# Kernel tuning notes

Hardware: AMD Instinct MI355X
Metric: run time of the kernel (lower is better)

The kernel has to match this reference:

```python
import jax, jax.numpy as jnp
import numpy as np
from jax import lax

GEN_POLY = ("1111001", "1011011")  # rate 1/2, constraint length 7 (octal 171/133)


def build_trellis(gen_poly):
    """Feed-forward (non-recursive) convolutional trellis tables.

    State = shift-register contents, most-recent bit is the MSB of the state
    index. Returns int32 tables, each [ns, ni]:
      to_nodes[s, b]        : next state from state s with input bit b
      op_by_fromnode[s, b]  : emitted output-symbol index for (s, b)
      from_nodes[j, m]      : m-th predecessor state of state j
      ip_by_tonode[j, m]    : input bit taken on that predecessor transition
    """
    mu = len(gen_poly[0]) - 1
    ns, ni = 2 ** mu, 2
    g = np.array([[int(c) for c in p] for p in gen_poly])  # [conv_n, mu+1]
    to_nodes = np.zeros((ns, ni), np.int32)
    op_by_fromnode = np.zeros((ns, ni), np.int32)
    from_nodes = np.zeros((ns, ni), np.int32)
    ip_by_tonode = np.zeros((ns, ni), np.int32)
    fill = np.zeros(ns, np.int32)
    for s in range(ns):
        rbits = [(s >> (mu - 1 - j)) & 1 for j in range(mu)]
        for b in range(ni):
            w = np.array([b] + rbits)                 # full window [b, r0..r_{mu-1}]
            obits = (g @ w) % 2                        # output bits, MSB first
            o = int("".join(str(int(x)) for x in obits), 2)
            j = int("".join(str(x) for x in ([b] + rbits[:-1])), 2)
            to_nodes[s, b] = j
            op_by_fromnode[s, b] = o
            from_nodes[j, fill[j]] = s
            ip_by_tonode[j, fill[j]] = b
            fill[j] += 1
    return to_nodes, op_by_fromnode, from_nodes, ip_by_tonode


TO_NODES, OP_BY_FROM, FROM_NODES, IP_BY_TO = build_trellis(GEN_POLY)
CONV_N = len(GEN_POLY)
MU = len(GEN_POLY[0]) - 1
NS = 2 ** MU
NO = 2 ** CONV_N
# output-symbol bit patterns, MSB first, mapped to signs (1-2*bit)
_OP_BITS = np.array([[(o >> (CONV_N - 1 - j)) & 1 for j in range(CONV_N)]
                     for o in range(NO)], np.float32)
OP_SIGN = jnp.asarray(1.0 - 2.0 * _OP_BITS)  # [NO, CONV_N]
IP_SIGN = jnp.asarray([1.0, -1.0])           # sign of input bit b: 1-2b


def setup_inputs() -> dict:
    key = jax.random.key(0)
    k1, k2 = jax.random.split(key)
    B, n = 256, 4096
    T = n // CONV_N  # = k = 2048 info bits
    llr_ch = jax.random.normal(k1, (B, n), dtype=jnp.float32)
    llr_a = jax.random.normal(k2, (B, T), dtype=jnp.float32)
    return {"llr_ch": llr_ch, "llr_a": llr_a}


def _bcjr(llr_ch, llr_a):
    B, n = llr_ch.shape
    T = n // CONV_N
    # branch metrics: bm[t, b, o] = exp(0.5 * sum_j llr[b, t, j] * (1-2*opbit_j(o)))
    llr_r = llr_ch.reshape(B, T, CONV_N)
    bm = jnp.exp(0.5 * jnp.einsum('btj,oj->tbo', llr_r, OP_SIGN))  # [T, B, NO]
    llr_a_t = llr_a.T  # [T, B]

    def gamma_fn(bm_t, la_t):
        # a-priori factor exp(0.5*llr_a*(1-2b)) times channel branch metric
        ap = jnp.exp(0.5 * la_t[:, None, None] * IP_SIGN[None, None, :])  # [B,1,2]
        return ap * bm_t[:, OP_BY_FROM]  # [B, NS, 2]

    alpha0 = jnp.zeros((B, NS), jnp.float32).at[:, 0].set(1.0)

    def fwd(alpha_prev, inp):
        bm_t, la_t = inp
        gam = gamma_fn(bm_t, la_t)                        # [B, NS, 2] by from-state
        ag = gam * alpha_prev[:, :, None]                  # alpha_{t} * gamma_t
        agt = ag[:, FROM_NODES, IP_BY_TO]                  # regroup by to-state
        alpha = agt.sum(-1)
        alpha = alpha / alpha.sum(-1, keepdims=True)       # normalize (as in TF code)
        return alpha, alpha_prev                            # emit alpha BEFORE step t

    _, alphas = lax.scan(fwd, alpha0, (bm, llr_a_t))       # alphas[t] = alpha_t, [T,B,NS]

    beta_T = jnp.full((B, NS), 1.0 / NS, jnp.float32)      # non-terminated: uniform

    def bwd(beta_next, inp):
        bm_t, la_t, alpha_t = inp
        gam = gamma_fn(bm_t, la_t)                         # [B, NS, 2]
        bg = gam * beta_next[:, TO_NODES]                  # gamma * beta_{t+1}(to)
        beta = bg.sum(-1)
        beta = beta / beta.sum(-1, keepdims=True)
        joint = alpha_t[:, :, None] * bg                   # APP per (state, bit)
        llr_t = jnp.log(joint[..., 0].sum(-1)) - jnp.log(joint[..., 1].sum(-1))
        return beta, llr_t

    _, llrs_rev = lax.scan(bwd, beta_T, (bm[::-1], llr_a_t[::-1], alphas[::-1]))
    return llrs_rev[::-1].T  # [B, T] soft LLRs (hard_out=False)


def reference(llr_ch, llr_a):
    return _bcjr(llr_ch, llr_a)
```

## Files before the change

### kernel.cpp

```cpp
#include <hip/hip_runtime.h>

#define T_LEN 2048
#define NSTATE 64
#define NCHUNK 32
#define CH_S 64
#define WARM 64
#define RK 16

template<int CTRL>
__device__ __forceinline__ float dpp_add(float v) {
    int r = __builtin_amdgcn_update_dpp(0, __float_as_int(v), CTRL, 0xF, 0xF, true);
    return v + __int_as_float(r);
}

__device__ __forceinline__ float dpp_sum_to63(float v) {
    v = dpp_add<0x111>(v);
    v = dpp_add<0x112>(v);
    v = dpp_add<0x114>(v);
    v = dpp_add<0x118>(v);
    v = dpp_add<0x142>(v);
    v = dpp_add<0x143>(v);
    return v;
}

__device__ __forceinline__ float wave_total(float v) {
    float s = dpp_sum_to63(v);
    return __int_as_float(__builtin_amdgcn_readlane(__float_as_int(s), 63));
}

__device__ __forceinline__ float pair_sum_xor1(float v) {
    int r = __builtin_amdgcn_update_dpp(0, __float_as_int(v), 0xB1, 0xF, 0xF, true);
    return v + __int_as_float(r);
}

__device__ __forceinline__ unsigned short bf16_of(float f) {
    return (unsigned short)((__float_as_uint(f) + 0x8000u) >> 16);
}


template<bool STORE>
__device__ __forceinline__ float fwd_group(float state,
                                           const float* __restrict__ chp,
                                           const float* __restrict__ lap,
                                           unsigned short* __restrict__ alds,
                                           int g, int t0, int lane,
                                           float kE, float k0, float k1,
                                           int fs0, bool fhi)
{
    #pragma unroll
    for (int h = 0; h < 2; ++h) {
        const int gb = g + 8 * h;
        const float4* c4 = (const float4*)(chp + 2 * gb);
        const float4* a4 = (const float4*)(lap + gb);
        float4 cc[4], aa[2];
        #pragma unroll
        for (int i = 0; i < 4; ++i) cc[i] = c4[i];
        #pragma unroll
        for (int i = 0; i < 2; ++i) aa[i] = a4[i];
        #pragma unroll
        for (int i = 0; i < 8; ++i) {
            float l0 = (i & 1) ? cc[i >> 1].z : cc[i >> 1].x;
            float l1 = (i & 1) ? cc[i >> 1].w : cc[i >> 1].y;
            float la = ((const float*)aa)[i];
            if (STORE) alds[(gb + i - t0) * NSTATE + lane] = bf16_of(state);
            float x   = fmaf(la, kE, fmaf(l0, k0, l1 * k1));
            float g0v = exp2f(x);
            float g1v = __builtin_amdgcn_rcpf(g0v);
            float s0  = pair_sum_xor1(state * g0v);
            float s1  = pair_sum_xor1(state * g1v);
            float a0  = __shfl(s0, fs0, 64);
            float a1  = __shfl(s1, fs0, 64);
            state = fhi ? a1 : a0;
        }
    }
    float s = wave_total(state);
    return state * __builtin_amdgcn_rcpf(s);
}

template<bool LLR>
__device__ __forceinline__ float bwd_group(float state,
                                           const float* __restrict__ chp,
                                           const float* __restrict__ lap,
                                           const unsigned short* __restrict__ alds,
                                           float* __restrict__ outp,
                                           int g, int t0, int lane,
                                           float kE, float k0, float k1,
                                           int bs0, int bs1)
{
    #pragma unroll
    for (int h = 1; h >= 0; --h) {
        const int gb = g + 8 * h;
        const float4* c4 = (const float4*)(chp + 2 * gb);
        const float4* a4 = (const float4*)(lap + gb);
        float4 cc[4], aa[2];
        #pragma unroll
        for (int i = 0; i < 4; ++i) cc[i] = c4[i];
        #pragma unroll
        for (int i = 0; i < 2; ++i) aa[i] = a4[i];
        float av[8];
        if (LLR) {
            #pragma unroll
            for (int i = 0; i < 8; ++i)
                av[i] = __uint_as_float(((unsigned)alds[(gb + i - t0) * NSTATE + lane]) << 16);
        }
        #pragma unroll
        for (int i = 7; i >= 0; --i) {
            float l0 = (i & 1) ? cc[i >> 1].z : cc[i >> 1].x;
            float l1 = (i & 1) ? cc[i >> 1].w : cc[i >> 1].y;
            float la = ((const float*)aa)[i];
            float x   = fmaf(la, kE, fmaf(l0, k0, l1 * k1));
            float g0v = exp2f(x);
            float g1v = __builtin_amdgcn_rcpf(g0v);
            float t0v = __shfl(state, bs0, 64);
            float t1v = __shfl(state, bs1, 64);
            float p0 = g0v * t0v;
            float p1 = g1v * t1v;
            if (LLR) {
                float na = dpp_sum_to63(av[i] * p0);
                float nb = dpp_sum_to63(av[i] * p1);
                float d  = (__log2f(na) - __log2f(nb)) * 0.6931471805599453f;
                if (lane == 63) outp[gb + i] = d;
            }
            state = p0 + p1;
        }
    }
    float s = wave_total(state);
    return state * __builtin_amdgcn_rcpf(s);
}

__global__ __launch_bounds__(128, 8)
void bcjr_fused_kernel(const float* __restrict__ llr_ch,
                       const float* __restrict__ llr_a,
                       float* __restrict__ out)
{
    __shared__ unsigned short alds[CH_S * NSTATE];

    const int lane  = threadIdx.x & 63;
    const int role  = threadIdx.x >> 6;
    const int unit  = blockIdx.x;
    const int chunk = unit & (NCHUNK - 1);
    const int b     = unit >> 5;

    const float c0 = 1.0f - 2.0f * (float)(__popc(lane & 57) & 1);
    const float c1 = 1.0f - 2.0f * (float)(__popc(lane & 27) & 1);
    const float kE = 0.5f * 1.442695040888963f;
    const float k0 = kE * c0, k1 = kE * c1;

    const float* chp = llr_ch + (size_t)b * (2 * T_LEN);
    const float* lap = llr_a  + (size_t)b * T_LEN;
    const int t0 = chunk * CH_S;

    if (role == 0) {
        const int  fs0 = 2 * (lane & 31);
        const bool fhi = (lane >= 32);
        float state = (chunk == 0) ? ((lane == 0) ? 1.0f : 0.0f) : (1.0f / 64.0f);
        const int ts = (chunk == 0) ? t0 : t0 - WARM;
        for (int g = ts; g < t0; g += RK)
            state = fwd_group<false>(state, chp, lap, alds, g, t0, lane, kE, k0, k1, fs0, fhi);
        for (int g = t0; g < t0 + CH_S; g += RK)
            state = fwd_group<true>(state, chp, lap, alds, g, t0, lane, kE, k0, k1, fs0, fhi);
        __syncthreads();
    } else {
        const int bs0 = lane >> 1;
        const int bs1 = 32 + (lane >> 1);
        float state = 1.0f / 64.0f;
        const int te = (chunk == NCHUNK - 1) ? (t0 + CH_S) : (t0 + CH_S + WARM);
        for (int g = te - RK; g >= t0 + CH_S; g -= RK)
            state = bwd_group<false>(state, chp, lap, alds, nullptr, g, t0, lane, kE, k0, k1, bs0, bs1);
        __syncthreads();
        float* outp = out + (size_t)b * T_LEN;
        for (int g = t0 + CH_S - RK; g >= t0; g -= RK)
            state = bwd_group<true>(state, chp, lap, alds, outp, g, t0, lane, kE, k0, k1, bs0, bs1);
    }
}

extern "C" void kernel_launch(void* const* d_in, const int* in_sizes, int n_in,
                              void* d_out, int out_size, void* d_ws, size_t ws_size,
                              hipStream_t stream) {
    const float* llr_ch = (const float*)d_in[0];
    const float* llr_a  = (const float*)d_in[1];
    float* out = (float*)d_out;

    int B = in_sizes[0] / (2 * T_LEN);
    (void)d_ws; (void)ws_size;

    int n_units = B * NCHUNK;
    hipLaunchKernelGGL(bcjr_fused_kernel, dim3(n_units), dim3(128), 0, stream,
                       llr_ch, llr_a, out);
}
```

Baseline: 141.4 us.

## Precompute gammas cooperatively per wave and broadcast via ds_bpermute, double larger chunks

Each lane now computes the branch metric exp2 and its reciprocal for one (timestep, output-symbol) pair across a 16-step group, since 64 lanes cover 16 steps times 4 symbols. The per-step recurrence then fetches its gamma values with ds_bpermute instead of recomputing exp2 per state lane. The channel loads are software-prefetched one group ahead, and the LLR reduction is restructured to combine both numerator and denominator in one shared reduction tree. Chunk size doubles to 128 with half as many blocks, which cuts warm-up overhead but lowers parallelism, and the occupancy hint drops to 4.

New measurement: 161.6 us. +14.2%, slower.

```diff
diff --git a/kernel.cpp b/kernel.cpp
--- a/kernel.cpp
+++ b/kernel.cpp
@@ -2,8 +2,8 @@
 
 #define T_LEN 2048
 #define NSTATE 64
-#define NCHUNK 32
-#define CH_S 64
+#define NCHUNK 16
+#define CH_S 128
 #define WARM 64
 #define RK 16
 
@@ -33,102 +33,100 @@
     return v + __int_as_float(r);
 }
 
+__device__ __forceinline__ float bperm(int addrb, float v) {
+    return __int_as_float(__builtin_amdgcn_ds_bpermute(addrb, __float_as_int(v)));
+}
+
 __device__ __forceinline__ unsigned short bf16_of(float f) {
     return (unsigned short)((__float_as_uint(f) + 0x8000u) >> 16);
 }
 
 
+struct Ctx {
+    const float* chp;
+    const float* lap;
+    int tl;
+    int qb;
+    unsigned m0;
+    unsigned m1;
+};
+
+__device__ __forceinline__ void load_grp(const Ctx& c, int gg, float& la, float2& ch) {
+    la = c.lap[gg + c.tl];
+    ch = ((const float2*)c.chp)[gg + c.tl];
+}
+
+__device__ __forceinline__ void make_ER(const Ctx& c, float la, float2 ch,
+                                        float& E, float& R) {
+    const float kE = 0.5f * 1.442695040888963f;
+    float x0 = __uint_as_float(__float_as_uint(ch.x) ^ c.m0);
+    float x1 = __uint_as_float(__float_as_uint(ch.y) ^ c.m1);
+    float xv = kE * (la + x0 + x1);
+    E = exp2f(xv);
+    R = __builtin_amdgcn_rcpf(E);
+}
+
 template<bool STORE>
-__device__ __forceinline__ float fwd_group(float state,
-                                           const float* __restrict__ chp,
-                                           const float* __restrict__ lap,
-                                           unsigned short* __restrict__ alds,
-                                           int g, int t0, int lane,
-                                           float kE, float k0, float k1,
-                                           int fs0, bool fhi)
-{
+__device__ __forceinline__ float fwd_group(const Ctx& c, float state, float E, float R,
+                                           unsigned short* alds, int g, int t0,
+                                           int lane, int fselb) {
     #pragma unroll
-    for (int h = 0; h < 2; ++h) {
-        const int gb = g + 8 * h;
-        const float4* c4 = (const float4*)(chp + 2 * gb);
-        const float4* a4 = (const float4*)(lap + gb);
-        float4 cc[4], aa[2];
-        #pragma unroll
-        for (int i = 0; i < 4; ++i) cc[i] = c4[i];
-        #pragma unroll
-        for (int i = 0; i < 2; ++i) aa[i] = a4[i];
-        #pragma unroll
-        for (int i = 0; i < 8; ++i) {
-            float l0 = (i & 1) ? cc[i >> 1].z : cc[i >> 1].x;
-            float l1 = (i & 1) ? cc[i >> 1].w : cc[i >> 1].y;
-            float la = ((const float*)aa)[i];
-            if (STORE) alds[(gb + i - t0) * NSTATE + lane] = bf16_of(state);
-            float x   = fmaf(la, kE, fmaf(l0, k0, l1 * k1));
-            float g0v = exp2f(x);
-            float g1v = __builtin_amdgcn_rcpf(g0v);
-            float s0  = pair_sum_xor1(state * g0v);
-            float s1  = pair_sum_xor1(state * g1v);
-            float a0  = __shfl(s0, fs0, 64);
-            float a1  = __shfl(s1, fs0, 64);
-            state = fhi ? a1 : a0;
-        }
+    for (int i = 0; i < RK; ++i) {
+        if (STORE) alds[(g + i - t0) * NSTATE + lane] = bf16_of(state);
+        int ab = c.qb + (i << 4);
+        float g0v = bperm(ab, E);
+        float g1v = bperm(ab, R);
+        float s0 = pair_sum_xor1(state * g0v);
+        float s1 = pair_sum_xor1(state * g1v);
+        float v  = (lane & 1) ? s1 : s0;
+        state = bperm(fselb, v);
     }
     float s = wave_total(state);
     return state * __builtin_amdgcn_rcpf(s);
 }
 
 template<bool LLR>
-__device__ __forceinline__ float bwd_group(float state,
-                                           const float* __restrict__ chp,
-                                           const float* __restrict__ lap,
-                                           const unsigned short* __restrict__ alds,
-                                           float* __restrict__ outp,
+__device__ __forceinline__ float bwd_group(const Ctx& c, float state, float E, float R,
+                                           const unsigned short* alds, float* outp,
                                            int g, int t0, int lane,
-                                           float kE, float k0, float k1,
-                                           int bs0, int bs1)
-{
+                                           int bs0b, int bs1b) {
+    float av[RK];
+    if (LLR) {
+        #pragma unroll
+        for (int i = 0; i < RK; ++i)
+            av[i] = __uint_as_float(((unsigned)alds[(g + i - t0) * NSTATE + lane]) << 16);
+    }
     #pragma unroll
-    for (int h = 1; h >= 0; --h) {
-        const int gb = g + 8 * h;
-        const float4* c4 = (const float4*)(chp + 2 * gb);
-        const float4* a4 = (const float4*)(lap + gb);
-        float4 cc[4], aa[2];
-        #pragma unroll
-        for (int i = 0; i < 4; ++i) cc[i] = c4[i];
-        #pragma unroll
-        for (int i = 0; i < 2; ++i) aa[i] = a4[i];
-        float av[8];
+    for (int i = RK - 1; i >= 0; --i) {
+        int ab = c.qb + (i << 4);
+        float g0v = bperm(ab, E);
+        float g1v = bperm(ab, R);
+        float t0v = bperm(bs0b, state);
+        float t1v = bperm(bs1b, state);
+        float p0 = g0v * t0v;
+        float p1 = g1v * t1v;
         if (LLR) {
-            #pragma unroll
-            for (int i = 0; i < 8; ++i)
-                av[i] = __uint_as_float(((unsigned)alds[(gb + i - t0) * NSTATE + lane]) << 16);
-        }
-        #pragma unroll
-        for (int i = 7; i >= 0; --i) {
-            float l0 = (i & 1) ? cc[i >> 1].z : cc[i >> 1].x;
-            float l1 = (i & 1) ? cc[i >> 1].w : cc[i >> 1].y;
-            float la = ((const float*)aa)[i];
-            float x   = fmaf(la, kE, fmaf(l0, k0, l1 * k1));
-            float g0v = exp2f(x);
-            float g1v = __builtin_amdgcn_rcpf(g0v);
-            float t0v = __shfl(state, bs0, 64);
-            float t1v = __shfl(state, bs1, 64);
-            float p0 = g0v * t0v;
-            float p1 = g1v * t1v;
-            if (LLR) {
-                float na = dpp_sum_to63(av[i] * p0);
-                float nb = dpp_sum_to63(av[i] * p1);
-                float d  = (__log2f(na) - __log2f(nb)) * 0.6931471805599453f;
-                if (lane == 63) outp[gb + i] = d;
-            }
-            state = p0 + p1;
-        }
+            float na = av[i] * p0;
+            float nb = av[i] * p1;
+            na += __shfl_xor(na, 32, 64);
+            nb += __shfl_xor(nb, 32, 64);
+            float z = (lane >= 32) ? nb : na;
+            z = dpp_add<0xB1>(z);
+            z = dpp_add<0x4E>(z);
+            z = dpp_add<0x124>(z);
+            z = dpp_add<0x128>(z);
+            z += __shfl_xor(z, 16, 64);
+            float lg = __log2f(z);
+            float d  = (lg - __shfl_xor(lg, 32, 64)) * 0.6931471805599453f;
+            if (lane == 0) outp[g + i] = d;
+        }
+        state = p0 + p1;
     }
     float s = wave_total(state);
     return state * __builtin_amdgcn_rcpf(s);
 }
 
-__global__ __launch_bounds__(128, 8)
+__global__ __launch_bounds__(128, 4)
 void bcjr_fused_kernel(const float* __restrict__ llr_ch,
                        const float* __restrict__ llr_a,
                        float* __restrict__ out)
@@ -139,38 +137,60 @@
     const int role  = threadIdx.x >> 6;
     const int unit  = blockIdx.x;
     const int chunk = unit & (NCHUNK - 1);
-    const int b     = unit >> 5;
-
-    const float c0 = 1.0f - 2.0f * (float)(__popc(lane & 57) & 1);
-    const float c1 = 1.0f - 2.0f * (float)(__popc(lane & 27) & 1);
-    const float kE = 0.5f * 1.442695040888963f;
-    const float k0 = kE * c0, k1 = kE * c1;
-
-    const float* chp = llr_ch + (size_t)b * (2 * T_LEN);
-    const float* lap = llr_a  + (size_t)b * T_LEN;
+    const int b     = unit >> 4;
+
+    Ctx c;
+    c.chp = llr_ch + (size_t)b * (2 * T_LEN);
+    c.lap = llr_a  + (size_t)b * T_LEN;
+    c.tl  = lane >> 2;
+    c.m0  = (unsigned)(lane & 1) << 31;
+    c.m1  = (unsigned)((lane >> 1) & 1) << 31;
+    const int q = (__popc(lane & 57) & 1) | ((__popc(lane & 27) & 1) << 1);
+    c.qb  = q << 2;
     const int t0 = chunk * CH_S;
 
     if (role == 0) {
-        const int  fs0 = 2 * (lane & 31);
-        const bool fhi = (lane >= 32);
+        const int fselb = (2 * (lane & 31) + (lane >> 5)) << 2;
         float state = (chunk == 0) ? ((lane == 0) ? 1.0f : 0.0f) : (1.0f / 64.0f);
-        const int ts = (chunk == 0) ? t0 : t0 - WARM;
-        for (int g = ts; g < t0; g += RK)
-            state = fwd_group<false>(state, chp, lap, alds, g, t0, lane, kE, k0, k1, fs0, fhi);
-        for (int g = t0; g < t0 + CH_S; g += RK)
-            state = fwd_group<true>(state, chp, lap, alds, g, t0, lane, kE, k0, k1, fs0, fhi);
+        const int ts   = (chunk == 0) ? t0 : t0 - WARM;
+        const int tend = t0 + CH_S;
+        float laC; float2 chC;
+        load_grp(c, ts, laC, chC);
+        for (int g = ts; g < tend; g += RK) {
+            int gn = (g + RK < tend) ? g + RK : g;
+            float laN; float2 chN;
+            load_grp(c, gn, laN, chN);
+            float E, R; make_ER(c, laC, chC, E, R);
+            if (g < t0) state = fwd_group<false>(c, state, E, R, alds, g, t0, lane, fselb);
+            else        state = fwd_group<true >(c, state, E, R, alds, g, t0, lane, fselb);
+            laC = laN; chC = chN;
+        }
         __syncthreads();
     } else {
-        const int bs0 = lane >> 1;
-        const int bs1 = 32 + (lane >> 1);
+        const int bs0b = (lane >> 1) << 2;
+        const int bs1b = bs0b + 128;
         float state = 1.0f / 64.0f;
         const int te = (chunk == NCHUNK - 1) ? (t0 + CH_S) : (t0 + CH_S + WARM);
-        for (int g = te - RK; g >= t0 + CH_S; g -= RK)
-            state = bwd_group<false>(state, chp, lap, alds, nullptr, g, t0, lane, kE, k0, k1, bs0, bs1);
+        float* outp = out + (size_t)b * T_LEN;
+        float laC; float2 chC;
+        load_grp(c, te - RK, laC, chC);
+        for (int g = te - RK; g >= t0 + CH_S; g -= RK) {
+            int gn = (g - RK >= t0) ? g - RK : g;
+            float laN; float2 chN;
+            load_grp(c, gn, laN, chN);
+            float E, R; make_ER(c, laC, chC, E, R);
+            state = bwd_group<false>(c, state, E, R, alds, nullptr, g, t0, lane, bs0b, bs1b);
+            laC = laN; chC = chN;
+        }
         __syncthreads();
-        float* outp = out + (size_t)b * T_LEN;
-        for (int g = t0 + CH_S - RK; g >= t0; g -= RK)
-            state = bwd_group<true>(state, chp, lap, alds, outp, g, t0, lane, kE, k0, k1, bs0, bs1);
+        for (int g = t0 + CH_S - RK; g >= t0; g -= RK) {
+            int gn = (g - RK >= t0) ? g - RK : g;
+            float laN; float2 chN;
+            load_grp(c, gn, laN, chN);
+            float E, R; make_ER(c, laC, chC, E, R);
+            state = bwd_group<true>(c, state, E, R, alds, outp, g, t0, lane, bs0b, bs1b);
+            laC = laN; chC = chN;
+        }
     }
 }
 
```

## Halve chunk count, use single bpermute in trellis steps, merge LLR reductions

Applied to the files above, without the earlier changes.

Doubles the chunk length to 128 steps with 16 chunks per batch row, which halves the redundant warm-up recursion relative to useful work but also halves the number of blocks. Replaces the two shuffles per step in the forward pass with one ds_bpermute on a lane-selected value. In the backward pass it uses one bpermute plus a DPP xor-1 move, with a sign flip on the exponent so odd lanes get the swapped gamma. It also merges the two 64-lane LLR reductions into one packed reduction across wave halves. The larger chunk doubles LDS usage per block and lengthens the serial path per block.

Result: slower. 163.0 us (+15.3%).

```diff
diff --git a/kernel.cpp b/kernel.cpp
--- a/kernel.cpp
+++ b/kernel.cpp
@@ -2,8 +2,8 @@
 
 #define T_LEN 2048
 #define NSTATE 64
-#define NCHUNK 32
-#define CH_S 64
+#define NCHUNK 16
+#define CH_S 128
 #define WARM 64
 #define RK 16
 
@@ -11,6 +11,10 @@
 __device__ __forceinline__ float dpp_add(float v) {
     int r = __builtin_amdgcn_update_dpp(0, __float_as_int(v), CTRL, 0xF, 0xF, true);
     return v + __int_as_float(r);
+}
+
+__device__ __forceinline__ float dpp_mov_xor1(float v) {
+    return __int_as_float(__builtin_amdgcn_update_dpp(0, __float_as_int(v), 0xB1, 0xF, 0xF, true));
 }
 
 __device__ __forceinline__ float dpp_sum_to63(float v) {
@@ -33,6 +37,10 @@
     return v + __int_as_float(r);
 }
 
+__device__ __forceinline__ float bperm(int addrb, float v) {
+    return __int_as_float(__builtin_amdgcn_ds_bpermute(addrb, __float_as_int(v)));
+}
+
 __device__ __forceinline__ unsigned short bf16_of(float f) {
     return (unsigned short)((__float_as_uint(f) + 0x8000u) >> 16);
 }
@@ -45,7 +53,7 @@
                                            unsigned short* __restrict__ alds,
                                            int g, int t0, int lane,
                                            float kE, float k0, float k1,
-                                           int fs0, bool fhi)
+                                           int fselb)
 {
     #pragma unroll
     for (int h = 0; h < 2; ++h) {
@@ -68,9 +76,8 @@
             float g1v = __builtin_amdgcn_rcpf(g0v);
             float s0  = pair_sum_xor1(state * g0v);
             float s1  = pair_sum_xor1(state * g1v);
-            float a0  = __shfl(s0, fs0, 64);
-            float a1  = __shfl(s1, fs0, 64);
-            state = fhi ? a1 : a0;
+            float v   = (lane & 1) ? s1 : s0;
+            state = bperm(fselb, v);
         }
     }
     float s = wave_total(state);
@@ -85,8 +92,9 @@
                                            float* __restrict__ outp,
                                            int g, int t0, int lane,
                                            float kE, float k0, float k1,
-                                           int bs0, int bs1)
+                                           unsigned pmask, int bgb)
 {
+    const bool odd = (lane & 1);
     #pragma unroll
     for (int h = 1; h >= 0; --h) {
         const int gb = g + 8 * h;
@@ -108,20 +116,32 @@
             float l0 = (i & 1) ? cc[i >> 1].z : cc[i >> 1].x;
             float l1 = (i & 1) ? cc[i >> 1].w : cc[i >> 1].y;
             float la = ((const float*)aa)[i];
-            float x   = fmaf(la, kE, fmaf(l0, k0, l1 * k1));
-            float g0v = exp2f(x);
-            float g1v = __builtin_amdgcn_rcpf(g0v);
-            float t0v = __shfl(state, bs0, 64);
-            float t1v = __shfl(state, bs1, 64);
-            float p0 = g0v * t0v;
-            float p1 = g1v * t1v;
+            float x  = fmaf(la, kE, fmaf(l0, k0, l1 * k1));
+            float xg = __uint_as_float(__float_as_uint(x) ^ pmask);
+            float ga = exp2f(xg);
+            float gb_ = __builtin_amdgcn_rcpf(ga);
+            float a  = bperm(bgb, state);
+            float bb = dpp_mov_xor1(a);
+            float u0 = ga * a;
+            float u1 = gb_ * bb;
             if (LLR) {
-                float na = dpp_sum_to63(av[i] * p0);
-                float nb = dpp_sum_to63(av[i] * p1);
-                float d  = (__log2f(na) - __log2f(nb)) * 0.6931471805599453f;
-                if (lane == 63) outp[gb + i] = d;
+                float p0 = odd ? u1 : u0;
+                float p1 = odd ? u0 : u1;
+                float na = av[i] * p0;
+                float nb = av[i] * p1;
+                na += __shfl_xor(na, 32, 64);
+                nb += __shfl_xor(nb, 32, 64);
+                float z = (lane >= 32) ? nb : na;
+                z = dpp_add<0xB1>(z);
+                z = dpp_add<0x4E>(z);
+                z = dpp_add<0x124>(z);
+                z = dpp_add<0x128>(z);
+                z += __shfl_xor(z, 16, 64);
+                float lg = __log2f(z);
+                float d  = (lg - __shfl_xor(lg, 32, 64)) * 0.6931471805599453f;
+                if (lane == 0) outp[gb + i] = d;
             }
-            state = p0 + p1;
+            state = u0 + u1;
         }
     }
     float s = wave_total(state);
@@ -139,7 +159,7 @@
     const int role  = threadIdx.x >> 6;
     const int unit  = blockIdx.x;
     const int chunk = unit & (NCHUNK - 1);
-    const int b     = unit >> 5;
+    const int b     = unit >> 4;
 
     const float c0 = 1.0f - 2.0f * (float)(__popc(lane & 57) & 1);
     const float c1 = 1.0f - 2.0f * (float)(__popc(lane & 27) & 1);
@@ -151,26 +171,25 @@
     const int t0 = chunk * CH_S;
 
     if (role == 0) {
-        const int  fs0 = 2 * (lane & 31);
-        const bool fhi = (lane >= 32);
+        const int fselb = (2 * (lane & 31) + (lane >> 5)) << 2;
         float state = (chunk == 0) ? ((lane == 0) ? 1.0f : 0.0f) : (1.0f / 64.0f);
         const int ts = (chunk == 0) ? t0 : t0 - WARM;
         for (int g = ts; g < t0; g += RK)
-            state = fwd_group<false>(state, chp, lap, alds, g, t0, lane, kE, k0, k1, fs0, fhi);
+            state = fwd_group<false>(state, chp, lap, alds, g, t0, lane, kE, k0, k1, fselb);
         for (int g = t0; g < t0 + CH_S; g += RK)
-            state = fwd_group<true>(state, chp, lap, alds, g, t0, lane, kE, k0, k1, fs0, fhi);
+            state = fwd_group<true>(state, chp, lap, alds, g, t0, lane, kE, k0, k1, fselb);
         __syncthreads();
     } else {
-        const int bs0 = lane >> 1;
-        const int bs1 = 32 + (lane >> 1);
+        const unsigned pmask = (unsigned)(lane & 1) << 31;
+        const int bgb = ((lane >> 1) + ((lane & 1) << 5)) << 2;
         float state = 1.0f / 64.0f;
         const int te = (chunk == NCHUNK - 1) ? (t0 + CH_S) : (t0 + CH_S + WARM);
         for (int g = te - RK; g >= t0 + CH_S; g -= RK)
-            state = bwd_group<false>(state, chp, lap, alds, nullptr, g, t0, lane, kE, k0, k1, bs0, bs1);
+            state = bwd_group<false>(state, chp, lap, alds, nullptr, g, t0, lane, kE, k0, k1, pmask, bgb);
         __syncthreads();
         float* outp = out + (size_t)b * T_LEN;
         for (int g = t0 + CH_S - RK; g >= t0; g -= RK)
-            state = bwd_group<true>(state, chp, lap, alds, outp, g, t0, lane, kE, k0, k1, bs0, bs1);
+            state = bwd_group<true>(state, chp, lap, alds, outp, g, t0, lane, kE, k0, k1, pmask, bgb);
     }
 }
 
```
